# Kernel tuning notes

Measured on AMD Instinct MI355X. Metric: run time of the kernel, lower is better.

The kernel has to match this reference:

```python
import jax, jax.numpy as jnp
import numpy as np

B, C_IN, C_OUT, N, MODES = 16, 128, 128, 16384, 128

def setup_inputs() -> dict:
    key = jax.random.key(0)
    k1, k2, k3, k4 = jax.random.split(key, 4)
    scale = 1.0 / (C_IN * C_OUT)
    x = jax.random.normal(k1, (B, C_IN, N), dtype=jnp.float32)
    wbases = jax.random.normal(k2, (N, MODES), dtype=jnp.float32)
    bases = jax.random.normal(k3, (N, MODES), dtype=jnp.float32)
    W = scale * jax.random.uniform(k4, (C_IN, C_OUT, MODES), dtype=jnp.float32)
    return {"x": x, "wbases": wbases, "bases": bases, "W": W}

def reference(x, wbases, bases, W):
    # project onto weighted bases: [B, C_in, N] x [N, K] -> [B, C_in, K]
    x_co = jnp.einsum('bcx,xk->bck', x, wbases)
    # per-mode channel mixing: [B, C_in, K] x [C_in, C_out, K] -> [B, C_out, K]
    x_hat = jnp.einsum('bik,iok->bok', x_co, W)
    # reconstruct: [B, C_out, K] x [N, K] -> [B, C_out, N]
    return jnp.einsum('bok,xk->box', x_hat, bases)
```

## Files before the change

### kernel.cpp

```cpp
#include <hip/hip_runtime.h>
#include <hip/hip_bf16.h>
#include <stdint.h>

#define NB 16
#define NC 128
#define NK 128
#define NSP 16384
#define SPLIT 32
#define CHUNK 512
#define BK 64

typedef float f32x4 __attribute__((ext_vector_type(4)));
typedef __bf16 bf16x8 __attribute__((ext_vector_type(8)));

__device__ __forceinline__ unsigned short f32_to_bf16(float a) {
  unsigned int u = __float_as_uint(a);
  return (unsigned short)((u + 0x7fffu + ((u >> 16) & 1u)) >> 16);
}

__device__ __forceinline__ unsigned int pack_bf16(float a, float b) {
  unsigned int ua = __float_as_uint(a);
  unsigned int ub = __float_as_uint(b);
  ua = (ua + 0x7fffu + ((ua >> 16) & 1u)) >> 16;
  ub = (ub + 0x7fffu + ((ub >> 16) & 1u)) & 0xffff0000u;
  return ua | ub;
}

__device__ __forceinline__ void gl_lds16(const void* g, void* l) {
  __builtin_amdgcn_global_load_lds(
      (const __attribute__((address_space(1))) unsigned int*)g,
      (__attribute__((address_space(3))) unsigned int*)l, 16, 0, 0);
}

__global__ void k0a_transpose(const float* __restrict__ wb,
                              unsigned short* __restrict__ wbT) {
  __shared__ float tile[32][33];
  int kt = (blockIdx.x & 3) * 32;
  int nt = (blockIdx.x >> 2) * 32;
  int tx = threadIdx.x & 31;
  int ty = threadIdx.x >> 5;
#pragma unroll
  for (int i = 0; i < 32; i += 8)
    tile[ty + i][tx] = wb[(size_t)(nt + ty + i) * NK + kt + tx];
  __syncthreads();
#pragma unroll
  for (int i = 0; i < 32; i += 8)
    wbT[(size_t)(kt + ty + i) * NSP + nt + tx] = f32_to_bf16(tile[tx][ty + i]);
}

__global__ void k0b_convert(const float* __restrict__ bases,
                            unsigned short* __restrict__ bb) {
  int i = blockIdx.x * 256 + threadIdx.x;
  if (i >= (NSP * NK) / 4) return;
  float4 v = ((const float4*)bases)[i];
  uint2 o;
  o.x = pack_bf16(v.x, v.y);
  o.y = pack_bf16(v.z, v.w);
  ((uint2*)bb)[i] = o;
}

__global__ __launch_bounds__(512, 4)
void k1_proj(const float* __restrict__ x, const unsigned short* __restrict__ wbT,
             float* __restrict__ part) {
  int blk = blockIdx.x;
  int b = blk >> 5;
  int chunk = blk & 31;
  int n0 = chunk * CHUNK;
  __shared__ unsigned short ldsA[8 * 128 * 8];
  __shared__ unsigned short ldsB[8320];
  int tid = threadIdx.x;
  int lane = tid & 63;
  int wave = tid >> 6;
  int cb = (wave & 1) * 64;
  int kb = (wave >> 1) * 32;
  int r = lane & 15;
  int q = lane >> 4;

  f32x4 acc[4][2];
#pragma unroll
  for (int t = 0; t < 4; ++t)
#pragma unroll
    for (int u = 0; u < 2; ++u) acc[t][u] = (f32x4){0.f, 0.f, 0.f, 0.f};

  int g = tid & 7;
  int row0 = tid >> 3;
  const float* xbase = x + (size_t)(b * NC) * NSP + n0 + g * 8;
  uint4* wA = (uint4*)ldsA;
  const bf16x8* pA = (const bf16x8*)ldsA;

  const unsigned short* wsrc =
      wbT + n0 + (size_t)(lane >> 3) * NSP + (lane & 7) * 8;

  for (int it = 0; it < CHUNK / BK; ++it) {
#pragma unroll
    for (int j = 0; j < 2; ++j) {
      int i = wave * 2 + j;
      gl_lds16(wsrc + (size_t)(i * 8) * NSP + it * BK, (char*)ldsB + i * 1040);
    }
#pragma unroll
    for (int jj = 0; jj < 2; ++jj) {
      int row = row0 + jj * 64;
      const float4* p = (const float4*)(xbase + (size_t)row * NSP + it * BK);
      float4 a0 = p[0];
      float4 a1 = p[1];
      uint4 u;
      u.x = pack_bf16(a0.x, a0.y);
      u.y = pack_bf16(a0.z, a0.w);
      u.z = pack_bf16(a1.x, a1.y);
      u.w = pack_bf16(a1.z, a1.w);
      wA[g * 128 + row] = u;
    }
    __syncthreads();
#pragma unroll
    for (int s = 0; s < 2; ++s) {
      bf16x8 af[4], bf[2];
#pragma unroll
      for (int t = 0; t < 4; ++t) af[t] = pA[(s * 4 + q) * 128 + cb + 16 * t + r];
#pragma unroll
      for (int u = 0; u < 2; ++u) {
        int rw = kb + 16 * u + r;
        bf[u] = *(const bf16x8*)((const char*)ldsB + rw * 128 + (rw >> 3) * 16 +
                                 s * 64 + q * 16);
      }
#pragma unroll
      for (int t = 0; t < 4; ++t)
#pragma unroll
        for (int u = 0; u < 2; ++u)
          acc[t][u] = __builtin_amdgcn_mfma_f32_16x16x32_bf16(af[t], bf[u],
                                                              acc[t][u], 0, 0, 0);
    }
    __syncthreads();
  }

  float* pp = part + (size_t)blk * (NC * NK);
  int rq = q * 4;
#pragma unroll
  for (int t = 0; t < 4; ++t)
#pragma unroll
    for (int u = 0; u < 2; ++u)
#pragma unroll
      for (int v = 0; v < 4; ++v)
        pp[(cb + 16 * t + rq + v) * NK + kb + 16 * u + r] = acc[t][u][v];
}

__global__ __launch_bounds__(256)
void k1b_reduce(const float* __restrict__ part, float* __restrict__ x_co) {
  int idx = blockIdx.x * 256 + threadIdx.x;
  int b = idx >> 13;
  int r2 = idx & 8191;
  const float2* p = (const float2*)(part + (size_t)b * SPLIT * (NC * NK)) + r2;
  float2 s = {0.f, 0.f};
#pragma unroll
  for (int c = 0; c < SPLIT; ++c) {
    float2 v = p[(size_t)c * (NC * NK / 2)];
    s.x += v.x;
    s.y += v.y;
  }
  ((float2*)x_co)[idx] = s;
}

__global__ __launch_bounds__(128)
void k2_mix(const float* __restrict__ x_co, const float* __restrict__ W,
            unsigned short* __restrict__ xhat_bf) {
  int b = blockIdx.x >> 7;
  int o = blockIdx.x & 127;
  int k = threadIdx.x;
  const float* xc = x_co + (size_t)b * NC * NK + k;
  const float* wp = W + (size_t)o * NK + k;
  float acc = 0.f;
#pragma unroll 4
  for (int i = 0; i < NC; ++i)
    acc += xc[(size_t)i * NK] * wp[(size_t)i * (NC * NK)];
  xhat_bf[((size_t)b * NC + o) * NK + k] = f32_to_bf16(acc);
}

__global__ __launch_bounds__(256, 2)
void k3_recon(const unsigned short* __restrict__ xhat_bf,
              const unsigned short* __restrict__ bases_bf,
              float* __restrict__ out) {
  int blk = blockIdx.x;
  int mo0 = (blk & 15) * 128;
  int n0 = (blk >> 4) * 512;
  __shared__ unsigned short ldsB[2][16640];
  int tid = threadIdx.x;
  int lane = tid & 63;
  int wave = tid >> 6;
  int mb = (wave & 1) * 64;
  int nb = (wave >> 1) * 64;
  int r = lane & 15;
  int q = lane >> 4;

  bf16x8 af[4][4];
#pragma unroll
  for (int t = 0; t < 4; ++t)
#pragma unroll
    for (int s = 0; s < 4; ++s)
      af[t][s] = *(const bf16x8*)(xhat_bf +
                                  (size_t)(mo0 + mb + 16 * t + r) * NK +
                                  s * 32 + q * 8);

  const unsigned short* bsrc =
      bases_bf + ((size_t)n0 + (lane >> 4)) * NK + (lane & 15) * 8;

#pragma unroll
  for (int jj = 0; jj < 8; ++jj) {
    int i = wave * 8 + jj;
    gl_lds16(bsrc + (size_t)(i * 4) * NK, (char*)ldsB[0] + i * 1040);
  }

  for (int sub = 0; sub < 4; ++sub) {
    __syncthreads();
    int cur = sub & 1;
    if (sub < 3) {
#pragma unroll
      for (int jj = 0; jj < 8; ++jj) {
        int i = wave * 8 + jj;
        gl_lds16(bsrc + (size_t)((sub + 1) * 128 + i * 4) * NK,
                 (char*)ldsB[cur ^ 1] + i * 1040);
      }
    }
    const char* bbuf = (const char*)ldsB[cur];
    f32x4 acc[4][4];
#pragma unroll
    for (int t = 0; t < 4; ++t)
#pragma unroll
      for (int u = 0; u < 4; ++u) acc[t][u] = (f32x4){0.f, 0.f, 0.f, 0.f};
#pragma unroll
    for (int s = 0; s < 4; ++s) {
      bf16x8 bf[4];
#pragma unroll
      for (int u = 0; u < 4; ++u) {
        int rw = nb + 16 * u + r;
        bf[u] = *(const bf16x8*)(bbuf + rw * 256 + (rw >> 2) * 16 + s * 64 +
                                 q * 16);
      }
#pragma unroll
      for (int t = 0; t < 4; ++t)
#pragma unroll
        for (int u = 0; u < 4; ++u)
          acc[t][u] = __builtin_amdgcn_mfma_f32_16x16x32_bf16(af[t][s], bf[u],
                                                              acc[t][u], 0, 0, 0);
    }
    int rq = q * 4;
#pragma unroll
    for (int t = 0; t < 4; ++t)
#pragma unroll
      for (int u = 0; u < 4; ++u)
#pragma unroll
        for (int v = 0; v < 4; ++v)
          out[(size_t)(mo0 + mb + 16 * t + rq + v) * NSP + n0 + sub * 128 +
              nb + 16 * u + r] = acc[t][u][v];
  }
}

extern "C" void kernel_launch(void* const* d_in, const int* in_sizes, int n_in,
                              void* d_out, int out_size, void* d_ws, size_t ws_size,
                              hipStream_t stream) {
  const float* x = (const float*)d_in[0];
  const float* wbases = (const float*)d_in[1];
  const float* bases = (const float*)d_in[2];
  const float* W = (const float*)d_in[3];
  float* out = (float*)d_out;

  char* ws = (char*)d_ws;
  if (ws_size < ((size_t)42 << 20)) return;
  unsigned short* wbT = (unsigned short*)(ws);
  unsigned short* bases_bf = (unsigned short*)(ws + ((size_t)4 << 20));
  float* part = (float*)(ws + ((size_t)8 << 20));
  float* x_co = (float*)(ws + ((size_t)40 << 20));
  unsigned short* xhat_bf = (unsigned short*)(ws + ((size_t)41 << 20));

  k0a_transpose<<<2048, 256, 0, stream>>>(wbases, wbT);
  k0b_convert<<<2048, 256, 0, stream>>>(bases, bases_bf);
  k1_proj<<<NB * SPLIT, 512, 0, stream>>>(x, wbT, part);
  k1b_reduce<<<512, 256, 0, stream>>>(part, x_co);
  k2_mix<<<NB * NC, 128, 0, stream>>>(x_co, W, xhat_bf);
  k3_recon<<<512, 256, 0, stream>>>(xhat_bf, bases_bf, out);
}
```

Before: 299.2 us.

## Double-buffer projection GEMM, XOR-swizzle LDS, merge prep kernels, two outputs per mix block

The projection kernel now double-buffers both its x tile and its wbT tile in LDS. The next tile's global loads are issued before the MFMA loop and the bf16 packing happens after it, so fetch latency overlaps compute. Both GEMM kernels replace padded LDS rows with an XOR swizzle on the global-to-LDS copy address to avoid bank conflicts without padding. The two prep kernels are merged into one launch, and the mixing kernel computes two output channels per block so each x_co load is reused. In exchange, the projection kernel uses more LDS and registers, which may lower occupancy.

```diff
diff --git a/kernel.cpp b/kernel.cpp
--- a/kernel.cpp
+++ b/kernel.cpp
@@ -32,31 +32,30 @@
       (__attribute__((address_space(3))) unsigned int*)l, 16, 0, 0);
 }
 
-__global__ void k0a_transpose(const float* __restrict__ wb,
-                              unsigned short* __restrict__ wbT) {
+__global__ void k0_prep(const float* __restrict__ wb, unsigned short* __restrict__ wbT,
+                        const float* __restrict__ bases, unsigned short* __restrict__ bb) {
   __shared__ float tile[32][33];
-  int kt = (blockIdx.x & 3) * 32;
-  int nt = (blockIdx.x >> 2) * 32;
-  int tx = threadIdx.x & 31;
-  int ty = threadIdx.x >> 5;
-#pragma unroll
-  for (int i = 0; i < 32; i += 8)
-    tile[ty + i][tx] = wb[(size_t)(nt + ty + i) * NK + kt + tx];
-  __syncthreads();
-#pragma unroll
-  for (int i = 0; i < 32; i += 8)
-    wbT[(size_t)(kt + ty + i) * NSP + nt + tx] = f32_to_bf16(tile[tx][ty + i]);
-}
-
-__global__ void k0b_convert(const float* __restrict__ bases,
-                            unsigned short* __restrict__ bb) {
-  int i = blockIdx.x * 256 + threadIdx.x;
-  if (i >= (NSP * NK) / 4) return;
-  float4 v = ((const float4*)bases)[i];
-  uint2 o;
-  o.x = pack_bf16(v.x, v.y);
-  o.y = pack_bf16(v.z, v.w);
-  ((uint2*)bb)[i] = o;
+  if (blockIdx.x < 2048) {
+    int bid = blockIdx.x;
+    int kt = (bid & 3) * 32;
+    int nt = (bid >> 2) * 32;
+    int tx = threadIdx.x & 31;
+    int ty = threadIdx.x >> 5;
+#pragma unroll
+    for (int i = 0; i < 32; i += 8)
+      tile[ty + i][tx] = wb[(size_t)(nt + ty + i) * NK + kt + tx];
+    __syncthreads();
+#pragma unroll
+    for (int i = 0; i < 32; i += 8)
+      wbT[(size_t)(kt + ty + i) * NSP + nt + tx] = f32_to_bf16(tile[tx][ty + i]);
+  } else {
+    int i = (blockIdx.x - 2048) * 256 + threadIdx.x;
+    float4 v = ((const float4*)bases)[i];
+    uint2 o;
+    o.x = pack_bf16(v.x, v.y);
+    o.y = pack_bf16(v.z, v.w);
+    ((uint2*)bb)[i] = o;
+  }
 }
 
 __global__ __launch_bounds__(512, 4)
@@ -66,8 +65,8 @@
   int b = blk >> 5;
   int chunk = blk & 31;
   int n0 = chunk * CHUNK;
-  __shared__ unsigned short ldsA[8 * 128 * 8];
-  __shared__ unsigned short ldsB[8320];
+  __shared__ unsigned short ldsA[2][8 * 128 * 8];
+  __shared__ unsigned short ldsB[2][128 * 64];
   int tid = threadIdx.x;
   int lane = tid & 63;
   int wave = tid >> 6;
@@ -85,22 +84,21 @@
   int g = tid & 7;
   int row0 = tid >> 3;
   const float* xbase = x + (size_t)(b * NC) * NSP + n0 + g * 8;
-  uint4* wA = (uint4*)ldsA;
-  const bf16x8* pA = (const bf16x8*)ldsA;
 
   const unsigned short* wsrc =
-      wbT + n0 + (size_t)(lane >> 3) * NSP + (lane & 7) * 8;
-
-  for (int it = 0; it < CHUNK / BK; ++it) {
-#pragma unroll
-    for (int j = 0; j < 2; ++j) {
-      int i = wave * 2 + j;
-      gl_lds16(wsrc + (size_t)(i * 8) * NSP + it * BK, (char*)ldsB + i * 1040);
-    }
+      wbT + n0 + (size_t)(lane >> 3) * NSP + ((lane & 7) ^ (lane >> 3)) * 8;
+
+#pragma unroll
+  for (int j = 0; j < 2; ++j) {
+    int i = wave * 2 + j;
+    gl_lds16(wsrc + (size_t)(i * 8) * NSP, (char*)ldsB[0] + i * 1024);
+  }
+  {
+    uint4* wA = (uint4*)ldsA[0];
 #pragma unroll
     for (int jj = 0; jj < 2; ++jj) {
       int row = row0 + jj * 64;
-      const float4* p = (const float4*)(xbase + (size_t)row * NSP + it * BK);
+      const float4* p = (const float4*)(xbase + (size_t)row * NSP);
       float4 a0 = p[0];
       float4 a1 = p[1];
       uint4 u;
@@ -110,17 +108,40 @@
       u.w = pack_bf16(a1.z, a1.w);
       wA[g * 128 + row] = u;
     }
-    __syncthreads();
+  }
+  __syncthreads();
+
+  for (int it = 0; it < CHUNK / BK; ++it) {
+    int cur = it & 1;
+    bool pf = (it + 1) < (CHUNK / BK);
+    float4 a0[2], a1[2];
+    if (pf) {
+#pragma unroll
+      for (int j = 0; j < 2; ++j) {
+        int i = wave * 2 + j;
+        gl_lds16(wsrc + (size_t)(i * 8) * NSP + (it + 1) * BK,
+                 (char*)ldsB[cur ^ 1] + i * 1024);
+      }
+#pragma unroll
+      for (int jj = 0; jj < 2; ++jj) {
+        int row = row0 + jj * 64;
+        const float4* p = (const float4*)(xbase + (size_t)row * NSP + (it + 1) * BK);
+        a0[jj] = p[0];
+        a1[jj] = p[1];
+      }
+    }
+    const bf16x8* pA = (const bf16x8*)ldsA[cur];
+    const char* pB = (const char*)ldsB[cur];
 #pragma unroll
     for (int s = 0; s < 2; ++s) {
       bf16x8 af[4], bf[2];
-#pragma unroll
-      for (int t = 0; t < 4; ++t) af[t] = pA[(s * 4 + q) * 128 + cb + 16 * t + r];
+      int s4q = s * 4 + q;
+#pragma unroll
+      for (int t = 0; t < 4; ++t) af[t] = pA[s4q * 128 + cb + 16 * t + r];
 #pragma unroll
       for (int u = 0; u < 2; ++u) {
         int rw = kb + 16 * u + r;
-        bf[u] = *(const bf16x8*)((const char*)ldsB + rw * 128 + (rw >> 3) * 16 +
-                                 s * 64 + q * 16);
+        bf[u] = *(const bf16x8*)(pB + rw * 128 + ((s4q ^ (r & 7)) << 4));
       }
 #pragma unroll
       for (int t = 0; t < 4; ++t)
@@ -128,6 +149,19 @@
         for (int u = 0; u < 2; ++u)
           acc[t][u] = __builtin_amdgcn_mfma_f32_16x16x32_bf16(af[t], bf[u],
                                                               acc[t][u], 0, 0, 0);
+    }
+    if (pf) {
+      uint4* wA = (uint4*)ldsA[cur ^ 1];
+#pragma unroll
+      for (int jj = 0; jj < 2; ++jj) {
+        int row = row0 + jj * 64;
+        uint4 u;
+        u.x = pack_bf16(a0[jj].x, a0[jj].y);
+        u.y = pack_bf16(a0[jj].z, a0[jj].w);
+        u.z = pack_bf16(a1[jj].x, a1[jj].y);
+        u.w = pack_bf16(a1[jj].z, a1[jj].w);
+        wA[g * 128 + row] = u;
+      }
     }
     __syncthreads();
   }
@@ -162,16 +196,21 @@
 __global__ __launch_bounds__(128)
 void k2_mix(const float* __restrict__ x_co, const float* __restrict__ W,
             unsigned short* __restrict__ xhat_bf) {
-  int b = blockIdx.x >> 7;
-  int o = blockIdx.x & 127;
+  int b = blockIdx.x >> 6;
+  int o0 = (blockIdx.x & 63) * 2;
   int k = threadIdx.x;
   const float* xc = x_co + (size_t)b * NC * NK + k;
-  const float* wp = W + (size_t)o * NK + k;
-  float acc = 0.f;
+  const float* w0 = W + (size_t)o0 * NK + k;
+  float a0 = 0.f, a1 = 0.f;
 #pragma unroll 4
-  for (int i = 0; i < NC; ++i)
-    acc += xc[(size_t)i * NK] * wp[(size_t)i * (NC * NK)];
-  xhat_bf[((size_t)b * NC + o) * NK + k] = f32_to_bf16(acc);
+  for (int i = 0; i < NC; ++i) {
+    float v = xc[(size_t)i * NK];
+    a0 += v * w0[(size_t)i * (NC * NK)];
+    a1 += v * w0[(size_t)i * (NC * NK) + NK];
+  }
+  size_t base = ((size_t)b * NC + o0) * NK + k;
+  xhat_bf[base] = f32_to_bf16(a0);
+  xhat_bf[base + NK] = f32_to_bf16(a1);
 }
 
 __global__ __launch_bounds__(256, 2)
@@ -181,7 +220,7 @@
   int blk = blockIdx.x;
   int mo0 = (blk & 15) * 128;
   int n0 = (blk >> 4) * 512;
-  __shared__ unsigned short ldsB[2][16640];
+  __shared__ unsigned short ldsB[2][128 * 128];
   int tid = threadIdx.x;
   int lane = tid & 63;
   int wave = tid >> 6;
@@ -199,13 +238,15 @@
                                   (size_t)(mo0 + mb + 16 * t + r) * NK +
                                   s * 32 + q * 8);
 
-  const unsigned short* bsrc =
-      bases_bf + ((size_t)n0 + (lane >> 4)) * NK + (lane & 15) * 8;
+  int rlane = lane >> 4;
+  int slane = lane & 15;
 
 #pragma unroll
   for (int jj = 0; jj < 8; ++jj) {
     int i = wave * 8 + jj;
-    gl_lds16(bsrc + (size_t)(i * 4) * NK, (char*)ldsB[0] + i * 1040);
+    int c = slane ^ (((i & 3) << 2) | rlane);
+    gl_lds16(bases_bf + (size_t)(n0 + i * 4 + rlane) * NK + c * 8,
+             (char*)ldsB[0] + i * 1024);
   }
 
   for (int sub = 0; sub < 4; ++sub) {
@@ -215,8 +256,9 @@
 #pragma unroll
       for (int jj = 0; jj < 8; ++jj) {
         int i = wave * 8 + jj;
-        gl_lds16(bsrc + (size_t)((sub + 1) * 128 + i * 4) * NK,
-                 (char*)ldsB[cur ^ 1] + i * 1040);
+        int c = slane ^ (((i & 3) << 2) | rlane);
+        gl_lds16(bases_bf + (size_t)(n0 + (sub + 1) * 128 + i * 4 + rlane) * NK + c * 8,
+                 (char*)ldsB[cur ^ 1] + i * 1024);
       }
     }
     const char* bbuf = (const char*)ldsB[cur];
@@ -228,11 +270,11 @@
 #pragma unroll
     for (int s = 0; s < 4; ++s) {
       bf16x8 bf[4];
+      int s4q = s * 4 + q;
 #pragma unroll
       for (int u = 0; u < 4; ++u) {
         int rw = nb + 16 * u + r;
-        bf[u] = *(const bf16x8*)(bbuf + rw * 256 + (rw >> 2) * 16 + s * 64 +
-                                 q * 16);
+        bf[u] = *(const bf16x8*)(bbuf + rw * 256 + ((s4q ^ r) << 4));
       }
 #pragma unroll
       for (int t = 0; t < 4; ++t)
@@ -270,10 +312,9 @@
   float* x_co = (float*)(ws + ((size_t)40 << 20));
   unsigned short* xhat_bf = (unsigned short*)(ws + ((size_t)41 << 20));
 
-  k0a_transpose<<<2048, 256, 0, stream>>>(wbases, wbT);
-  k0b_convert<<<2048, 256, 0, stream>>>(bases, bases_bf);
+  k0_prep<<<4096, 256, 0, stream>>>(wbases, wbT, bases, bases_bf);
   k1_proj<<<NB * SPLIT, 512, 0, stream>>>(x, wbT, part);
   k1b_reduce<<<512, 256, 0, stream>>>(part, x_co);
-  k2_mix<<<NB * NC, 128, 0, stream>>>(x_co, W, xhat_bf);
+  k2_mix<<<NB * NC / 2, 128, 0, stream>>>(x_co, W, xhat_bf);
   k3_recon<<<512, 256, 0, stream>>>(xhat_bf, bases_bf, out);
 }
```

New measurement: 300.2 us. No clear change (+0.4%).
